# Kernel optimization log

Measured on AMD Instinct MI355X. Metric: run time of the kernel, lower is better.

The kernel has to match this reference:

```python
import jax, jax.numpy as jnp
import numpy as np

IN_DIM = 1024
HID = 256
OUT_DIM = 1000
NUM_BINS = 51
BATCH = 2048
N_LEGAL = 200


def setup_inputs() -> dict:
    key = jax.random.key(0)
    ks = jax.random.split(key, 12)
    s = lambda fan_in: 1.0 / np.sqrt(fan_in)
    u = lambda k, shp, b: jax.random.uniform(k, shp, jnp.float32, -b, b)
    return {
        "x": jax.random.normal(ks[0], (BATCH, IN_DIM), jnp.float32),
        # weights stored as [in, out] (math-equivalent to torch Linear)
        "w_in": u(ks[1], (IN_DIM, HID), s(IN_DIM)),
        "b_in": u(ks[2], (HID,), s(IN_DIM)),
        "w_ah": u(ks[3], (HID, HID), s(HID)),
        "b_ah": u(ks[4], (HID,), s(HID)),
        "w_ao": u(ks[5], (HID, OUT_DIM * NUM_BINS), s(HID)),
        "b_ao": u(ks[6], (OUT_DIM * NUM_BINS,), s(HID)),
        "w_vh": u(ks[7], (HID, HID), s(HID)),
        "b_vh": u(ks[8], (HID,), s(HID)),
        "w_vo": u(ks[9], (HID, NUM_BINS), s(HID)),
        "b_vo": u(ks[10], (NUM_BINS,), s(HID)),
        "v_range": jnp.linspace(-10.0, 10.0, NUM_BINS, dtype=jnp.float32),
        "possible_moves": jax.random.randint(ks[11], (BATCH, N_LEGAL), 0, OUT_DIM),
    }


def reference(x, w_in, b_in, w_ah, b_ah, w_ao, b_ao, w_vh, b_vh, w_vo, b_vo,
              v_range, possible_moves):
    B = x.shape[0]
    h = jax.nn.relu(x @ w_in + b_in)                       # [B, 256]
    adv_h = jax.nn.relu(h @ w_ah + b_ah)                   # [B, 256]
    val_h = jax.nn.relu(h @ w_vh + b_vh)                   # [B, 256]
    adv = (adv_h @ w_ao + b_ao).reshape(B, OUT_DIM, NUM_BINS)
    val = (val_h @ w_vo + b_vo).reshape(B, 1, NUM_BINS)
    q = val + adv - adv.mean(axis=1, keepdims=True)        # [B, A, bins]
    p = jnp.maximum(jax.nn.softmax(q, axis=2), 1e-5)       # softmax + clamp(min=1e-5)
    q_vals = jnp.sum(p * v_range, axis=2)                  # [B, A]
    # LegalSoftmax: per-row scatter of 1.0 at legal indices, vectorized
    mask = jnp.zeros((B, OUT_DIM), x.dtype).at[
        jnp.arange(B)[:, None], possible_moves].set(1.0)
    filtered = q_vals * mask
    # faithful to torch: any exact-zero entry (masked OR coincidental) -> -inf
    return jnp.where(filtered == 0, -jnp.inf, filtered)
```

## Files before the change

kernel.cpp:

```cpp
#include <hip/hip_runtime.h>
#include <cstdint>
#include <cstddef>

#define NB      2048
#define INDIM   1024
#define HID     256
#define NA      1000
#define BINS    51
#define NLEG    200
#define NPAIR   (NB*NLEG)
#define NBLK    256
#define PPB     (NPAIR/NBLK)

#define NEG_SENTINEL (-1.0e30f)

typedef float    f32x4  __attribute__((ext_vector_type(4)));
typedef __bf16   bf16x8 __attribute__((ext_vector_type(8)));
typedef unsigned short us8 __attribute__((ext_vector_type(8)));
typedef unsigned long long u64x2 __attribute__((ext_vector_type(2)));

__device__ __forceinline__ unsigned short f2bf(float f) {
  union { float f; unsigned u; } v; v.f = f;
  return (unsigned short)((v.u + 0x7FFFu + ((v.u >> 16) & 1u)) >> 16);
}
__device__ __forceinline__ float bf2f(unsigned short h) {
  union { unsigned u; float f; } v; v.u = ((unsigned)h) << 16;
  return v.f;
}
__device__ __forceinline__ bf16x8 as_bf(us8 v) { return __builtin_bit_cast(bf16x8, v); }
__device__ __forceinline__ int imin(int a, int b) { return a < b ? a : b; }

__device__ __forceinline__ unsigned f2fp8x4(float a, float b, float c, float d) {
  int v = 0;
  v = __builtin_amdgcn_cvt_pk_fp8_f32(a, b, v, false);
  v = __builtin_amdgcn_cvt_pk_fp8_f32(c, d, v, true);
  return (unsigned)v;
}
__device__ __forceinline__ unsigned char f2fp8(float f) {
  int v = __builtin_amdgcn_cvt_pk_fp8_f32(f, 0.f, 0, false);
  return (unsigned char)(v & 0xff);
}
__device__ __forceinline__ float fp82f(unsigned char u) {
  return __builtin_amdgcn_cvt_f32_fp8((int)u, 0);
}

__global__ __launch_bounds__(256) void k_phase1(
    const float* __restrict__ w_ao, unsigned char* __restrict__ wp8,
    float* __restrict__ wmean_acc,
    const float* __restrict__ w_in, const float* __restrict__ w_ah,
    const float* __restrict__ w_vh,
    unsigned short* __restrict__ w_inT, unsigned short* __restrict__ w_ahT,
    unsigned short* __restrict__ w_vhT,
    float* __restrict__ out, const int* __restrict__ pm,
    int* __restrict__ hist) {
  __shared__ __align__(16) char smem[26240];
  int b = blockIdx.x, tid = threadIdx.x;
  if (b < 1000) {
    unsigned char* st = (unsigned char*)smem;
    int s = b & 7, a0 = (b >> 3) * 8;
    const float* wbase = w_ao + (size_t)(s * 32) * (NA * BINS) + a0 * BINS;
    for (int i = tid; i < 32 * 102; i += 256) {
      int r = i / 102, c4 = i - r * 102;
      float4 f = *(const float4*)(wbase + (size_t)r * (NA * BINS) + c4 * 4);
      *(unsigned*)(st + r * 420 + c4 * 4) =
          f2fp8x4(f.x * 16.f, f.y * 16.f, f.z * 16.f, f.w * 16.f);
    }
    __syncthreads();
    for (int i = tid; i < 32 * 51; i += 256) {
      int r = i / 51, j = i - r * 51;
      float s8 = 0.f;
#pragma unroll
      for (int aL = 0; aL < 8; aL++) s8 += fp82f(st[r * 420 + aL * 51 + j]);
      atomicAdd(&wmean_acc[(size_t)(s * 32 + r) * BINS + j], s8);
    }
    int t4 = (tid >> 6) & 3, l = tid & 63;
    int col = t4 * 16 + (l & 15), kg = l >> 4;
    for (int aL = 0; aL < 8; aL++) {
      unsigned lo = 0, hi = 0;
      if (col < BINS) {
        const unsigned char* p0 = st + (kg * 8) * 420 + aL * 51 + col;
        lo = (unsigned)p0[0] | ((unsigned)p0[420] << 8) |
             ((unsigned)p0[840] << 16) | ((unsigned)p0[1260] << 24);
        hi = (unsigned)p0[1680] | ((unsigned)p0[2100] << 8) |
             ((unsigned)p0[2520] << 16) | ((unsigned)p0[2940] << 24);
      }
      size_t fg = ((size_t)(a0 + aL) * 8 + s) * 4 + t4;
      uint2 v; v.x = lo; v.y = hi;
      *(uint2*)(wp8 + fg * 512 + (size_t)l * 8) = v;
    }
  } else if (b < 1884) {
    int bb = b - 1000;
    if (bb < 384) {
      float (*tile)[33] = (float(*)[33])smem;
      const float* w; unsigned short* wT; int K, N, kt, nt;
      if (bb < 256)      { w = w_in; wT = w_inT; K = INDIM; N = HID; kt = bb & 31;        nt = bb >> 5; }
      else if (bb < 320) { w = w_ah; wT = w_ahT; K = HID;   N = HID; kt = (bb - 256) & 7; nt = (bb - 256) >> 3; }
      else               { w = w_vh; wT = w_vhT; K = HID;   N = HID; kt = (bb - 320) & 7; nt = (bb - 320) >> 3; }
      int k0 = kt * 32, n0 = nt * 32;
      int cr = tid >> 5, cc = tid & 31;
#pragma unroll
      for (int it = 0; it < 4; it++)
        tile[cr + it * 8][cc] = w[(size_t)(k0 + cr + it * 8) * N + n0 + cc];
      __syncthreads();
#pragma unroll
      for (int it = 0; it < 4; it++)
        wT[(size_t)(n0 + cr + it * 8) * K + k0 + cc] = f2bf(tile[cc][cr + it * 8]);
    } else {
      int base = (bb - 384) * 1024 + tid;
      float4 v = {NEG_SENTINEL, NEG_SENTINEL, NEG_SENTINEL, NEG_SENTINEL};
#pragma unroll
      for (int it = 0; it < 4; it++) ((float4*)out)[base + it * 256] = v;
    }
  } else {
    int* lh = (int*)smem;
    int blk = b - 1884;
    for (int i = tid; i < NA; i += 256) lh[i] = 0;
    __syncthreads();
    int base = blk * PPB;
    for (int i = tid; i < PPB; i += 256) atomicAdd(&lh[pm[base + i]], 1);
    __syncthreads();
    for (int a = tid; a < NA; a += 256) hist[a * NBLK + blk] = lh[a];
  }
}

__global__ __launch_bounds__(256) void k_phase2(
    int* __restrict__ hist, int* __restrict__ cnt,
    const float* __restrict__ w_vo, const float* __restrict__ wmean_acc,
    const float* __restrict__ b_vo, const float* __restrict__ b_ao,
    unsigned short* __restrict__ Wc, float* __restrict__ bias_c,
    const float* __restrict__ x, const unsigned short* __restrict__ w_inT,
    const float* __restrict__ b_in, unsigned short* __restrict__ h_bf) {
  int b = blockIdx.x, tid = threadIdx.x;
  if (b < 1000) {
    __shared__ int s[256];
    int a = b, t = tid;
    int v = hist[a * NBLK + t];
    s[t] = v;
    __syncthreads();
    for (int d = 1; d < 256; d <<= 1) {
      int u = (t >= d) ? s[t - d] : 0;
      __syncthreads();
      s[t] += u;
      __syncthreads();
    }
    hist[a * NBLK + t] = s[t] - v;
    if (t == 255) cnt[a] = s[255];
  } else if (b < 1064) {
    __shared__ float s[256];
    int n = b - 1000, t = tid;
    for (int k = t; k < 512; k += 256) {
      float v = 0.f;
      if (n < BINS)
        v = (k < 256) ? w_vo[(size_t)k * BINS + n]
                      : (-(0.001f / 16.f) * wmean_acc[(size_t)(k - 256) * BINS + n]);
      Wc[(size_t)n * 512 + k] = f2bf(v);
    }
    float acc = 0.f;
    if (n < BINS)
      for (int a = t; a < NA; a += 256) acc += b_ao[(size_t)a * BINS + n];
    s[t] = acc;
    __syncthreads();
    for (int d = 128; d > 0; d >>= 1) { if (t < d) s[t] += s[t + d]; __syncthreads(); }
    if (t == 0) bias_c[n] = (n < BINS) ? (b_vo[n] - 0.001f * s[0]) : 0.f;
  } else {
    int w = tid >> 6, l = tid & 63, la = l & 15, g = l >> 4;
    int idx = (b - 1064) * 4 + w;
    int m0 = (idx & 127) * 16, n0 = (idx >> 7) * 16;
    f32x4 acc = {0.f, 0.f, 0.f, 0.f};
    const us8* Bp = (const us8*)(w_inT + (size_t)(n0 + la) * INDIM) + g;
    const float* Ar = x + (size_t)(m0 + la) * INDIM + g * 8;
    for (int s = 0; s < INDIM; s += 32) {
      float4 f0 = *(const float4*)(Ar + s);
      float4 f1 = *(const float4*)(Ar + s + 4);
      us8 u;
      u[0] = f2bf(f0.x); u[1] = f2bf(f0.y); u[2] = f2bf(f0.z); u[3] = f2bf(f0.w);
      u[4] = f2bf(f1.x); u[5] = f2bf(f1.y); u[6] = f2bf(f1.z); u[7] = f2bf(f1.w);
      acc = __builtin_amdgcn_mfma_f32_16x16x32_bf16(as_bf(u), as_bf(Bp[s >> 3]),
                                                    acc, 0, 0, 0);
    }
    float bb = b_in[n0 + la];
#pragma unroll
    for (int r = 0; r < 4; r++) {
      float v = fmaxf(acc[r] + bb, 0.f);
      h_bf[(size_t)(m0 + g * 4 + r) * HID + n0 + la] = f2bf(v);
    }
  }
}

__global__ __launch_bounds__(256) void k_phase3(
    const int* __restrict__ cnt, int* __restrict__ off,
    const unsigned short* __restrict__ h,
    const unsigned short* __restrict__ wA, const float* __restrict__ bA,
    unsigned char* __restrict__ Aext8, unsigned short* __restrict__ advh_bf,
    const unsigned short* __restrict__ wV, const float* __restrict__ bV,
    unsigned short* __restrict__ oV) {
  int b = blockIdx.x, tid = threadIdx.x;
  if (b == 1024) {
    __shared__ int s[256];
    int t = tid, i0 = 4 * t;
    int v0 = (i0     < NA) ? cnt[i0]     : 0;
    int v1 = (i0 + 1 < NA) ? cnt[i0 + 1] : 0;
    int v2 = (i0 + 2 < NA) ? cnt[i0 + 2] : 0;
    int v3 = (i0 + 3 < NA) ? cnt[i0 + 3] : 0;
    int sum = v0 + v1 + v2 + v3;
    s[t] = sum;
    __syncthreads();
    for (int d = 1; d < 256; d <<= 1) {
      int u = (t >= d) ? s[t - d] : 0;
      __syncthreads();
      s[t] += u;
      __syncthreads();
    }
    int excl = s[t] - sum;
    if (i0     < NA) off[i0]     = excl;
    if (i0 + 1 < NA) off[i0 + 1] = excl + v0;
    if (i0 + 2 < NA) off[i0 + 2] = excl + v0 + v1;
    if (i0 + 3 < NA) off[i0 + 3] = excl + v0 + v1 + v2;
  } else {
    int w = tid >> 6, l = tid & 63, la = l & 15, g = l >> 4;
    int idx = b * 4 + w;
    int m0 = (idx & 127) * 16;
    int ny = idx >> 7;
    int second = ny >> 4;
    int n0 = (ny & 15) * 16;
    const unsigned short* BT = second ? wV : wA;
    const float* bias = second ? bV : bA;
    f32x4 acc = {0.f, 0.f, 0.f, 0.f};
    const us8* Bp = (const us8*)(BT + (size_t)(n0 + la) * HID) + g;
    const us8* Ap = (const us8*)(h + (size_t)(m0 + la) * HID) + g;
#pragma unroll
    for (int s = 0; s < 8; s++)
      acc = __builtin_amdgcn_mfma_f32_16x16x32_bf16(as_bf(Ap[s * 4]), as_bf(Bp[s * 4]),
                                                    acc, 0, 0, 0);
    float bb = bias[n0 + la];
#pragma unroll
    for (int r = 0; r < 4; r++) {
      float v = fmaxf(acc[r] + bb, 0.f);
      size_t o = (size_t)(m0 + g * 4 + r) * HID + n0 + la;
      if (second) {
        oV[o] = f2bf(v);
      } else {
        advh_bf[o] = f2bf(v);
        Aext8[o] = f2fp8(v);
      }
    }
  }
}

__global__ __launch_bounds__(256) void k_phase4(
    const int* __restrict__ pm, const int* __restrict__ off,
    const int* __restrict__ hist, int* __restrict__ rows,
    const unsigned short* __restrict__ valh, const unsigned short* __restrict__ advh,
    const unsigned short* __restrict__ Wc, const float* __restrict__ bias_c,
    unsigned short* __restrict__ cbuf) {
  int b = blockIdx.x, tid = threadIdx.x;
  if (b < 256) {
    __shared__ int lc[NA];
    __shared__ int lbase[NA];
    int blk = b, t = tid;
    for (int i = t; i < NA; i += 256) {
      lc[i] = 0;
      lbase[i] = off[i] + hist[i * NBLK + blk];
    }
    __syncthreads();
    int base = blk * PPB;
    for (int i = t; i < PPB; i += 256) {
      int a = pm[base + i];
      int r = atomicAdd(&lc[a], 1);
      rows[lbase[a] + r] = (base + i) / NLEG;
    }
  } else {
    int w = tid >> 6, l = tid & 63, la = l & 15, g = l >> 4;
    int idx = (b - 256) * 4 + w;
    int m0 = (idx & 127) * 16, n0 = (idx >> 7) * 16;
    f32x4 acc = {0.f, 0.f, 0.f, 0.f};
    const us8* Bp  = (const us8*)(Wc + (size_t)(n0 + la) * 512) + g;
    const us8* Ap1 = (const us8*)(valh + (size_t)(m0 + la) * HID) + g;
    const us8* Ap2 = (const us8*)(advh + (size_t)(m0 + la) * HID) + g;
#pragma unroll
    for (int s = 0; s < 8; s++)
      acc = __builtin_amdgcn_mfma_f32_16x16x32_bf16(as_bf(Ap1[s * 4]), as_bf(Bp[s * 4]),
                                                    acc, 0, 0, 0);
#pragma unroll
    for (int s = 0; s < 8; s++)
      acc = __builtin_amdgcn_mfma_f32_16x16x32_bf16(as_bf(Ap2[s * 4]), as_bf(Bp[(8 + s) * 4]),
                                                    acc, 0, 0, 0);
    float bb = bias_c[n0 + la];
#pragma unroll
    for (int r = 0; r < 4; r++)
      cbuf[(size_t)(m0 + g * 4 + r) * 64 + n0 + la] = f2bf(acc[r] + bb);
  }
}

__global__ __launch_bounds__(256) void k_main_mfma(
    const unsigned char* __restrict__ Aext8,
    const unsigned short* __restrict__ cbuf,
    const unsigned char* __restrict__ wp8,
    const float* __restrict__ b_ao,
    const float* __restrict__ v_range,
    const int* __restrict__ cnt, const int* __restrict__ off,
    const int* __restrict__ rows,
    float* __restrict__ out) {
  __shared__ __align__(16) long long sB8[2048];
  int bx = blockIdx.x;
  int a = (bx & 7) * 125 + (bx >> 3);
  int count = cnt[a];
  int ntiles = (count + 15) >> 4;
  if ((int)(blockIdx.y * 4) >= ntiles) return;
  int tid = threadIdx.x;
  const u64x2* wpa = (const u64x2*)(wp8 + (size_t)a * 16384);
  for (int i = tid; i < 1024; i += 256) ((u64x2*)sB8)[i] = wpa[i];
  __syncthreads();

  int w = tid >> 6, l = tid & 63, la = l & 15, g = l >> 4;
  int base = off[a];
  float vr[4], bao[4];
#pragma unroll
  for (int t = 0; t < 4; t++) {
    int bin = t * 16 + la;
    bool vb = bin < BINS;
    vr[t]  = vb ? v_range[bin] : 0.f;
    bao[t] = vb ? b_ao[(size_t)a * BINS + bin] : 0.f;
  }

  for (int tile = blockIdx.y * 4 + w; tile < ntiles; tile += 8) {
    int m16 = tile * 16;
    int rA = rows[base + imin(m16 + la, count - 1)];
    const long long* Ap = (const long long*)(Aext8 + (size_t)rA * HID) + g;
    const us8* Cp = (const us8*)(cbuf + (size_t)rA * 64) + g;
    f32x4 acc[4];
#pragma unroll
    for (int t = 0; t < 4; t++) acc[t] = (f32x4){0.f, 0.f, 0.f, 0.f};
#pragma unroll
    for (int s = 0; s < 8; s++) {
      long long a8 = Ap[s * 4];
#pragma unroll
      for (int t = 0; t < 4; t++)
        acc[t] = __builtin_amdgcn_mfma_f32_16x16x32_fp8_fp8(
            a8, sB8[(s * 4 + t) * 64 + l], acc[t], 0, 0, 0);
    }
    {
      us8 c0 = Cp[0], c1 = Cp[4];
#pragma unroll
      for (int t = 0; t < 4; t++) {
        int colg = t * 16 + la;
        us8 u0, u1;
#pragma unroll
        for (int j = 0; j < 8; j++) {
          u0[j] = (g * 8 + j == colg)      ? (unsigned short)0x4180 : (unsigned short)0;
          u1[j] = (g * 8 + j + 32 == colg) ? (unsigned short)0x4180 : (unsigned short)0;
        }
        acc[t] = __builtin_amdgcn_mfma_f32_16x16x32_bf16(as_bf(c0), as_bf(u0), acc[t], 0, 0, 0);
        acc[t] = __builtin_amdgcn_mfma_f32_16x16x32_bf16(as_bf(c1), as_bf(u1), acc[t], 0, 0, 0);
      }
    }
#pragma unroll
    for (int r = 0; r < 4; r++) {
      int gi = m16 + g * 4 + r;
      bool vrow = gi < count;
      int b = __shfl(rA, g * 4 + r, 16);
      float e[4];
      float S = 0.f;
#pragma unroll
      for (int t = 0; t < 4; t++) {
        int bin = t * 16 + la;
        float v = (bin < BINS) ? (acc[t][r] * 0.0625f + bao[t]) : -1.0e30f;
        e[t] = __expf(v);
        S += e[t];
      }
#pragma unroll
      for (int i = 1; i < 16; i <<= 1) S += __shfl_xor(S, i);
      float inv = 1.f / S;
      float qv = 0.f;
#pragma unroll
      for (int t = 0; t < 4; t++) {
        int bin = t * 16 + la;
        if (bin < BINS) qv = fmaf(fmaxf(e[t] * inv, 1e-5f), vr[t], qv);
      }
#pragma unroll
      for (int i = 1; i < 16; i <<= 1) qv += __shfl_xor(qv, i);
      if (vrow && la == 0)
        out[(size_t)b * NA + a] = (qv == 0.f) ? NEG_SENTINEL : qv;
    }
  }
}

extern "C" void kernel_launch(void* const* d_in, const int* in_sizes, int n_in,
                              void* d_out, int out_size, void* d_ws, size_t ws_size,
                              hipStream_t stream) {
  (void)in_sizes; (void)n_in; (void)out_size; (void)ws_size;
  const float* x     = (const float*)d_in[0];
  const float* w_in  = (const float*)d_in[1];
  const float* b_in  = (const float*)d_in[2];
  const float* w_ah  = (const float*)d_in[3];
  const float* b_ah  = (const float*)d_in[4];
  const float* w_ao  = (const float*)d_in[5];
  const float* b_ao  = (const float*)d_in[6];
  const float* w_vh  = (const float*)d_in[7];
  const float* b_vh  = (const float*)d_in[8];
  const float* w_vo  = (const float*)d_in[9];
  const float* b_vo  = (const float*)d_in[10];
  const float* v_rng = (const float*)d_in[11];
  const int*   pm    = (const int*)d_in[12];
  float* out = (float*)d_out;

  char* p = (char*)d_ws;
  unsigned char*  wp8     = (unsigned char*)p;  p += (size_t)NA * 32 * 512;
  unsigned char*  Aext8   = (unsigned char*)p;  p += (size_t)NB * HID;
  unsigned short* cbuf    = (unsigned short*)p; p += (size_t)NB * 64 * 2;
  unsigned short* h_bf    = (unsigned short*)p; p += (size_t)NB * HID * 2;
  unsigned short* advh_bf = (unsigned short*)p; p += (size_t)NB * HID * 2;
  unsigned short* valh_bf = (unsigned short*)p; p += (size_t)NB * HID * 2;
  unsigned short* w_inT   = (unsigned short*)p; p += (size_t)HID * INDIM * 2;
  unsigned short* w_ahT   = (unsigned short*)p; p += (size_t)HID * HID * 2;
  unsigned short* w_vhT   = (unsigned short*)p; p += (size_t)HID * HID * 2;
  unsigned short* Wc      = (unsigned short*)p; p += (size_t)64 * 512 * 2;
  float* bias_c = (float*)p; p += 64 * 4;
  float* wmean  = (float*)p; p += 13056 * 4;
  int* cnt  = (int*)p; p += NA * 4;
  int* off  = (int*)p; p += NA * 4;
  int* hist = (int*)p; p += (size_t)NA * NBLK * 4;
  int* rows = (int*)p; p += (size_t)NPAIR * 4 + 256;

  hipMemsetAsync(wmean, 0, 13056 * sizeof(float), stream);

  k_phase1<<<2140, 256, 0, stream>>>(w_ao, wp8, wmean, w_in, w_ah, w_vh,
                                     w_inT, w_ahT, w_vhT, out, pm, hist);
  k_phase2<<<1576, 256, 0, stream>>>(hist, cnt, w_vo, wmean, b_vo, b_ao,
                                     Wc, bias_c, x, w_inT, b_in, h_bf);
  k_phase3<<<1025, 256, 0, stream>>>(cnt, off, h_bf, w_ahT, b_ah, Aext8,
                                     advh_bf, w_vhT, b_vh, valh_bf);
  k_phase4<<<384, 256, 0, stream>>>(pm, off, hist, rows, valh_bf, advh_bf,
                                    Wc, bias_c, cbuf);
  k_main_mfma<<<dim3(1000, 2), 256, 0, stream>>>(Aext8, cbuf, wp8, b_ao, v_rng,
                                                 cnt, off, rows, out);
}
```

Measured before the change: 220.9 us.

## Merge phases to drop a launch and use fixed per-action row capacity

Moves the first-layer GEMM into phase1, reading fp32 w_in directly and converting it to bf16 on the fly instead of transposing it first. The hidden-layer GEMMs move into phase2, which removes one kernel launch and one grid-wide dependency. The per-action offset prefix scan is replaced by a fixed capacity of BCAP=576 rows per action. The main kernel also prefetches the next tile's row index. The fixed capacity assumes no action collects more than 576 legal pairs, which holds for the uniform random moves but would overflow on skewed inputs.

```diff
diff --git a/kernel.cpp b/kernel.cpp
--- a/kernel.cpp
+++ b/kernel.cpp
@@ -11,6 +11,7 @@
 #define NPAIR   (NB*NLEG)
 #define NBLK    256
 #define PPB     (NPAIR/NBLK)
+#define BCAP    576
 
 #define NEG_SENTINEL (-1.0e30f)
 
@@ -49,10 +50,11 @@
     float* __restrict__ wmean_acc,
     const float* __restrict__ w_in, const float* __restrict__ w_ah,
     const float* __restrict__ w_vh,
-    unsigned short* __restrict__ w_inT, unsigned short* __restrict__ w_ahT,
-    unsigned short* __restrict__ w_vhT,
+    unsigned short* __restrict__ w_ahT, unsigned short* __restrict__ w_vhT,
     float* __restrict__ out, const int* __restrict__ pm,
-    int* __restrict__ hist) {
+    int* __restrict__ hist,
+    const float* __restrict__ x, const float* __restrict__ b_in,
+    unsigned short* __restrict__ h_bf) {
   __shared__ __align__(16) char smem[26240];
   int b = blockIdx.x, tid = threadIdx.x;
   if (b < 1000) {
@@ -88,38 +90,60 @@
       uint2 v; v.x = lo; v.y = hi;
       *(uint2*)(wp8 + fg * 512 + (size_t)l * 8) = v;
     }
+  } else if (b < 1128) {
+    float (*tile)[33] = (float(*)[33])smem;
+    int bb = b - 1000;
+    const float* w = (bb < 64) ? w_ah : w_vh;
+    unsigned short* wT = (bb < 64) ? w_ahT : w_vhT;
+    int t6 = bb & 63;
+    int k0 = (t6 & 7) * 32, n0 = (t6 >> 3) * 32;
+    int cr = tid >> 5, cc = tid & 31;
+#pragma unroll
+    for (int it = 0; it < 4; it++)
+      tile[cr + it * 8][cc] = w[(size_t)(k0 + cr + it * 8) * HID + n0 + cc];
+    __syncthreads();
+#pragma unroll
+    for (int it = 0; it < 4; it++)
+      wT[(size_t)(n0 + cr + it * 8) * HID + k0 + cc] = f2bf(tile[cc][cr + it * 8]);
+  } else if (b < 1628) {
+    int base = (b - 1128) * 1024 + tid;
+    float4 v = {NEG_SENTINEL, NEG_SENTINEL, NEG_SENTINEL, NEG_SENTINEL};
+#pragma unroll
+    for (int it = 0; it < 4; it++) ((float4*)out)[base + it * 256] = v;
   } else if (b < 1884) {
-    int bb = b - 1000;
-    if (bb < 384) {
-      float (*tile)[33] = (float(*)[33])smem;
-      const float* w; unsigned short* wT; int K, N, kt, nt;
-      if (bb < 256)      { w = w_in; wT = w_inT; K = INDIM; N = HID; kt = bb & 31;        nt = bb >> 5; }
-      else if (bb < 320) { w = w_ah; wT = w_ahT; K = HID;   N = HID; kt = (bb - 256) & 7; nt = (bb - 256) >> 3; }
-      else               { w = w_vh; wT = w_vhT; K = HID;   N = HID; kt = (bb - 320) & 7; nt = (bb - 320) >> 3; }
-      int k0 = kt * 32, n0 = nt * 32;
-      int cr = tid >> 5, cc = tid & 31;
-#pragma unroll
-      for (int it = 0; it < 4; it++)
-        tile[cr + it * 8][cc] = w[(size_t)(k0 + cr + it * 8) * N + n0 + cc];
-      __syncthreads();
-#pragma unroll
-      for (int it = 0; it < 4; it++)
-        wT[(size_t)(n0 + cr + it * 8) * K + k0 + cc] = f2bf(tile[cc][cr + it * 8]);
-    } else {
-      int base = (bb - 384) * 1024 + tid;
-      float4 v = {NEG_SENTINEL, NEG_SENTINEL, NEG_SENTINEL, NEG_SENTINEL};
-#pragma unroll
-      for (int it = 0; it < 4; it++) ((float4*)out)[base + it * 256] = v;
-    }
-  } else {
     int* lh = (int*)smem;
-    int blk = b - 1884;
+    int blk = b - 1628;
     for (int i = tid; i < NA; i += 256) lh[i] = 0;
     __syncthreads();
     int base = blk * PPB;
     for (int i = tid; i < PPB; i += 256) atomicAdd(&lh[pm[base + i]], 1);
     __syncthreads();
     for (int a = tid; a < NA; a += 256) hist[a * NBLK + blk] = lh[a];
+  } else {
+    int w = tid >> 6, l = tid & 63, la = l & 15, g = l >> 4;
+    int idx = (b - 1884) * 4 + w;
+    int m0 = (idx & 127) * 16, n0 = (idx >> 7) * 16;
+    f32x4 acc = {0.f, 0.f, 0.f, 0.f};
+    const float* Ar = x + (size_t)(m0 + la) * INDIM + g * 8;
+    const float* Wc0 = w_in + (size_t)(g * 8) * HID + n0 + la;
+    for (int s = 0; s < INDIM; s += 32) {
+      float4 f0 = *(const float4*)(Ar + s);
+      float4 f1 = *(const float4*)(Ar + s + 4);
+      us8 u, v;
+      u[0] = f2bf(f0.x); u[1] = f2bf(f0.y); u[2] = f2bf(f0.z); u[3] = f2bf(f0.w);
+      u[4] = f2bf(f1.x); u[5] = f2bf(f1.y); u[6] = f2bf(f1.z); u[7] = f2bf(f1.w);
+      const float* Wk = Wc0 + (size_t)s * HID;
+#pragma unroll
+      for (int j = 0; j < 8; j++) v[j] = f2bf(Wk[(size_t)j * HID]);
+      acc = __builtin_amdgcn_mfma_f32_16x16x32_bf16(as_bf(u), as_bf(v),
+                                                    acc, 0, 0, 0);
+    }
+    float bb = b_in[n0 + la];
+#pragma unroll
+    for (int r = 0; r < 4; r++) {
+      float v = fmaxf(acc[r] + bb, 0.f);
+      h_bf[(size_t)(m0 + g * 4 + r) * HID + n0 + la] = f2bf(v);
+    }
   }
 }
 
@@ -128,8 +152,11 @@
     const float* __restrict__ w_vo, const float* __restrict__ wmean_acc,
     const float* __restrict__ b_vo, const float* __restrict__ b_ao,
     unsigned short* __restrict__ Wc, float* __restrict__ bias_c,
-    const float* __restrict__ x, const unsigned short* __restrict__ w_inT,
-    const float* __restrict__ b_in, unsigned short* __restrict__ h_bf) {
+    const unsigned short* __restrict__ h,
+    const unsigned short* __restrict__ wA, const float* __restrict__ bA,
+    unsigned char* __restrict__ Aext8, unsigned short* __restrict__ advh_bf,
+    const unsigned short* __restrict__ wV, const float* __restrict__ bV,
+    unsigned short* __restrict__ oV) {
   int b = blockIdx.x, tid = threadIdx.x;
   if (b < 1000) {
     __shared__ int s[256];
@@ -165,60 +192,6 @@
   } else {
     int w = tid >> 6, l = tid & 63, la = l & 15, g = l >> 4;
     int idx = (b - 1064) * 4 + w;
-    int m0 = (idx & 127) * 16, n0 = (idx >> 7) * 16;
-    f32x4 acc = {0.f, 0.f, 0.f, 0.f};
-    const us8* Bp = (const us8*)(w_inT + (size_t)(n0 + la) * INDIM) + g;
-    const float* Ar = x + (size_t)(m0 + la) * INDIM + g * 8;
-    for (int s = 0; s < INDIM; s += 32) {
-      float4 f0 = *(const float4*)(Ar + s);
-      float4 f1 = *(const float4*)(Ar + s + 4);
-      us8 u;
-      u[0] = f2bf(f0.x); u[1] = f2bf(f0.y); u[2] = f2bf(f0.z); u[3] = f2bf(f0.w);
-      u[4] = f2bf(f1.x); u[5] = f2bf(f1.y); u[6] = f2bf(f1.z); u[7] = f2bf(f1.w);
-      acc = __builtin_amdgcn_mfma_f32_16x16x32_bf16(as_bf(u), as_bf(Bp[s >> 3]),
-                                                    acc, 0, 0, 0);
-    }
-    float bb = b_in[n0 + la];
-#pragma unroll
-    for (int r = 0; r < 4; r++) {
-      float v = fmaxf(acc[r] + bb, 0.f);
-      h_bf[(size_t)(m0 + g * 4 + r) * HID + n0 + la] = f2bf(v);
-    }
-  }
-}
-
-__global__ __launch_bounds__(256) void k_phase3(
-    const int* __restrict__ cnt, int* __restrict__ off,
-    const unsigned short* __restrict__ h,
-    const unsigned short* __restrict__ wA, const float* __restrict__ bA,
-    unsigned char* __restrict__ Aext8, unsigned short* __restrict__ advh_bf,
-    const unsigned short* __restrict__ wV, const float* __restrict__ bV,
-    unsigned short* __restrict__ oV) {
-  int b = blockIdx.x, tid = threadIdx.x;
-  if (b == 1024) {
-    __shared__ int s[256];
-    int t = tid, i0 = 4 * t;
-    int v0 = (i0     < NA) ? cnt[i0]     : 0;
-    int v1 = (i0 + 1 < NA) ? cnt[i0 + 1] : 0;
-    int v2 = (i0 + 2 < NA) ? cnt[i0 + 2] : 0;
-    int v3 = (i0 + 3 < NA) ? cnt[i0 + 3] : 0;
-    int sum = v0 + v1 + v2 + v3;
-    s[t] = sum;
-    __syncthreads();
-    for (int d = 1; d < 256; d <<= 1) {
-      int u = (t >= d) ? s[t - d] : 0;
-      __syncthreads();
-      s[t] += u;
-      __syncthreads();
-    }
-    int excl = s[t] - sum;
-    if (i0     < NA) off[i0]     = excl;
-    if (i0 + 1 < NA) off[i0 + 1] = excl + v0;
-    if (i0 + 2 < NA) off[i0 + 2] = excl + v0 + v1;
-    if (i0 + 3 < NA) off[i0 + 3] = excl + v0 + v1 + v2;
-  } else {
-    int w = tid >> 6, l = tid & 63, la = l & 15, g = l >> 4;
-    int idx = b * 4 + w;
     int m0 = (idx & 127) * 16;
     int ny = idx >> 7;
     int second = ny >> 4;
@@ -247,9 +220,9 @@
   }
 }
 
-__global__ __launch_bounds__(256) void k_phase4(
-    const int* __restrict__ pm, const int* __restrict__ off,
-    const int* __restrict__ hist, int* __restrict__ rows,
+__global__ __launch_bounds__(256) void k_phase3(
+    const int* __restrict__ pm, const int* __restrict__ hist,
+    int* __restrict__ rows,
     const unsigned short* __restrict__ valh, const unsigned short* __restrict__ advh,
     const unsigned short* __restrict__ Wc, const float* __restrict__ bias_c,
     unsigned short* __restrict__ cbuf) {
@@ -260,7 +233,7 @@
     int blk = b, t = tid;
     for (int i = t; i < NA; i += 256) {
       lc[i] = 0;
-      lbase[i] = off[i] + hist[i * NBLK + blk];
+      lbase[i] = i * BCAP + hist[i * NBLK + blk];
     }
     __syncthreads();
     int base = blk * PPB;
@@ -298,7 +271,7 @@
     const unsigned char* __restrict__ wp8,
     const float* __restrict__ b_ao,
     const float* __restrict__ v_range,
-    const int* __restrict__ cnt, const int* __restrict__ off,
+    const int* __restrict__ cnt,
     const int* __restrict__ rows,
     float* __restrict__ out) {
   __shared__ __align__(16) long long sB8[2048];
@@ -313,7 +286,7 @@
   __syncthreads();
 
   int w = tid >> 6, l = tid & 63, la = l & 15, g = l >> 4;
-  int base = off[a];
+  int base = a * BCAP;
   float vr[4], bao[4];
 #pragma unroll
   for (int t = 0; t < 4; t++) {
@@ -323,9 +296,11 @@
     bao[t] = vb ? b_ao[(size_t)a * BINS + bin] : 0.f;
   }
 
-  for (int tile = blockIdx.y * 4 + w; tile < ntiles; tile += 8) {
-    int m16 = tile * 16;
-    int rA = rows[base + imin(m16 + la, count - 1)];
+  int tile = blockIdx.y * 4 + w;
+  int rA = rows[base + imin(tile * 16 + la, count - 1)];
+  for (; tile < ntiles; tile += 8) {
+    int tn = tile + 8;
+    int rAn = (tn < ntiles) ? rows[base + imin(tn * 16 + la, count - 1)] : 0;
     const long long* Ap = (const long long*)(Aext8 + (size_t)rA * HID) + g;
     const us8* Cp = (const us8*)(cbuf + (size_t)rA * 64) + g;
     f32x4 acc[4];
@@ -354,6 +329,7 @@
         acc[t] = __builtin_amdgcn_mfma_f32_16x16x32_bf16(as_bf(c1), as_bf(u1), acc[t], 0, 0, 0);
       }
     }
+    int m16 = tile * 16;
 #pragma unroll
     for (int r = 0; r < 4; r++) {
       int gi = m16 + g * 4 + r;
@@ -382,6 +358,7 @@
       if (vrow && la == 0)
         out[(size_t)b * NA + a] = (qv == 0.f) ? NEG_SENTINEL : qv;
     }
+    rA = rAn;
   }
 }
 
@@ -411,27 +388,25 @@
   unsigned short* h_bf    = (unsigned short*)p; p += (size_t)NB * HID * 2;
   unsigned short* advh_bf = (unsigned short*)p; p += (size_t)NB * HID * 2;
   unsigned short* valh_bf = (unsigned short*)p; p += (size_t)NB * HID * 2;
-  unsigned short* w_inT   = (unsigned short*)p; p += (size_t)HID * INDIM * 2;
   unsigned short* w_ahT   = (unsigned short*)p; p += (size_t)HID * HID * 2;
   unsigned short* w_vhT   = (unsigned short*)p; p += (size_t)HID * HID * 2;
   unsigned short* Wc      = (unsigned short*)p; p += (size_t)64 * 512 * 2;
   float* bias_c = (float*)p; p += 64 * 4;
   float* wmean  = (float*)p; p += 13056 * 4;
   int* cnt  = (int*)p; p += NA * 4;
-  int* off  = (int*)p; p += NA * 4;
   int* hist = (int*)p; p += (size_t)NA * NBLK * 4;
-  int* rows = (int*)p; p += (size_t)NPAIR * 4 + 256;
+  int* rows = (int*)p; p += (size_t)NA * BCAP * 4 + 256;
 
   hipMemsetAsync(wmean, 0, 13056 * sizeof(float), stream);
 
-  k_phase1<<<2140, 256, 0, stream>>>(w_ao, wp8, wmean, w_in, w_ah, w_vh,
-                                     w_inT, w_ahT, w_vhT, out, pm, hist);
-  k_phase2<<<1576, 256, 0, stream>>>(hist, cnt, w_vo, wmean, b_vo, b_ao,
-                                     Wc, bias_c, x, w_inT, b_in, h_bf);
-  k_phase3<<<1025, 256, 0, stream>>>(cnt, off, h_bf, w_ahT, b_ah, Aext8,
+  k_phase1<<<2396, 256, 0, stream>>>(w_ao, wp8, wmean, w_in, w_ah, w_vh,
+                                     w_ahT, w_vhT, out, pm, hist,
+                                     x, b_in, h_bf);
+  k_phase2<<<2088, 256, 0, stream>>>(hist, cnt, w_vo, wmean, b_vo, b_ao,
+                                     Wc, bias_c, h_bf, w_ahT, b_ah, Aext8,
                                      advh_bf, w_vhT, b_vh, valh_bf);
-  k_phase4<<<384, 256, 0, stream>>>(pm, off, hist, rows, valh_bf, advh_bf,
+  k_phase3<<<384, 256, 0, stream>>>(pm, hist, rows, valh_bf, advh_bf,
                                     Wc, bias_c, cbuf);
   k_main_mfma<<<dim3(1000, 2), 256, 0, stream>>>(Aext8, cbuf, wp8, b_ao, v_rng,
-                                                 cnt, off, rows, out);
-}
+                                                 cnt, rows, out);
+}
```

Measured after the change: 224.6 us. About the same (+1.7%).

## Use fixed-capacity per-action row buckets and merge main kernel blocks per action

Applied to the files above, without the earlier changes.

Each action gets a fixed slot of BCAP rows in the row list instead of an offset from a global exclusive scan. This removes the offset-scan block from phase3 and the `off` array. The main MFMA kernel now runs one block per action instead of two, so the per-action fp8 weight tile is staged into shared memory once, and the next tile's row index is prefetched. Phase1 and phase2 block roles are reordered so the GEMM and histogram work is dispatched before the cheaper tasks. The fixed capacity assumes no action has more than 576 legal rows, which holds only for random-looking inputs. The main kernel also loses half its blocks, which reduces parallelism.

```diff
diff --git a/kernel.cpp b/kernel.cpp
--- a/kernel.cpp
+++ b/kernel.cpp
@@ -11,6 +11,7 @@
 #define NPAIR   (NB*NLEG)
 #define NBLK    256
 #define PPB     (NPAIR/NBLK)
+#define BCAP    576
 
 #define NEG_SENTINEL (-1.0e30f)
 
@@ -88,38 +89,36 @@
       uint2 v; v.x = lo; v.y = hi;
       *(uint2*)(wp8 + fg * 512 + (size_t)l * 8) = v;
     }
-  } else if (b < 1884) {
+  } else if (b < 1384) {
+    float (*tile)[33] = (float(*)[33])smem;
     int bb = b - 1000;
-    if (bb < 384) {
-      float (*tile)[33] = (float(*)[33])smem;
-      const float* w; unsigned short* wT; int K, N, kt, nt;
-      if (bb < 256)      { w = w_in; wT = w_inT; K = INDIM; N = HID; kt = bb & 31;        nt = bb >> 5; }
-      else if (bb < 320) { w = w_ah; wT = w_ahT; K = HID;   N = HID; kt = (bb - 256) & 7; nt = (bb - 256) >> 3; }
-      else               { w = w_vh; wT = w_vhT; K = HID;   N = HID; kt = (bb - 320) & 7; nt = (bb - 320) >> 3; }
-      int k0 = kt * 32, n0 = nt * 32;
-      int cr = tid >> 5, cc = tid & 31;
-#pragma unroll
-      for (int it = 0; it < 4; it++)
-        tile[cr + it * 8][cc] = w[(size_t)(k0 + cr + it * 8) * N + n0 + cc];
-      __syncthreads();
-#pragma unroll
-      for (int it = 0; it < 4; it++)
-        wT[(size_t)(n0 + cr + it * 8) * K + k0 + cc] = f2bf(tile[cc][cr + it * 8]);
-    } else {
-      int base = (bb - 384) * 1024 + tid;
-      float4 v = {NEG_SENTINEL, NEG_SENTINEL, NEG_SENTINEL, NEG_SENTINEL};
-#pragma unroll
-      for (int it = 0; it < 4; it++) ((float4*)out)[base + it * 256] = v;
-    }
-  } else {
+    const float* w; unsigned short* wT; int K, N, kt, nt;
+    if (bb < 256)      { w = w_in; wT = w_inT; K = INDIM; N = HID; kt = bb & 31;        nt = bb >> 5; }
+    else if (bb < 320) { w = w_ah; wT = w_ahT; K = HID;   N = HID; kt = (bb - 256) & 7; nt = (bb - 256) >> 3; }
+    else               { w = w_vh; wT = w_vhT; K = HID;   N = HID; kt = (bb - 320) & 7; nt = (bb - 320) >> 3; }
+    int k0 = kt * 32, n0 = nt * 32;
+    int cr = tid >> 5, cc = tid & 31;
+#pragma unroll
+    for (int it = 0; it < 4; it++)
+      tile[cr + it * 8][cc] = w[(size_t)(k0 + cr + it * 8) * N + n0 + cc];
+    __syncthreads();
+#pragma unroll
+    for (int it = 0; it < 4; it++)
+      wT[(size_t)(n0 + cr + it * 8) * K + k0 + cc] = f2bf(tile[cc][cr + it * 8]);
+  } else if (b < 1640) {
     int* lh = (int*)smem;
-    int blk = b - 1884;
+    int blk = b - 1384;
     for (int i = tid; i < NA; i += 256) lh[i] = 0;
     __syncthreads();
     int base = blk * PPB;
     for (int i = tid; i < PPB; i += 256) atomicAdd(&lh[pm[base + i]], 1);
     __syncthreads();
     for (int a = tid; a < NA; a += 256) hist[a * NBLK + blk] = lh[a];
+  } else {
+    int base = (b - 1640) * 1024 + tid;
+    float4 v = {NEG_SENTINEL, NEG_SENTINEL, NEG_SENTINEL, NEG_SENTINEL};
+#pragma unroll
+    for (int it = 0; it < 4; it++) ((float4*)out)[base + it * 256] = v;
   }
 }
 
@@ -131,40 +130,9 @@
     const float* __restrict__ x, const unsigned short* __restrict__ w_inT,
     const float* __restrict__ b_in, unsigned short* __restrict__ h_bf) {
   int b = blockIdx.x, tid = threadIdx.x;
-  if (b < 1000) {
-    __shared__ int s[256];
-    int a = b, t = tid;
-    int v = hist[a * NBLK + t];
-    s[t] = v;
-    __syncthreads();
-    for (int d = 1; d < 256; d <<= 1) {
-      int u = (t >= d) ? s[t - d] : 0;
-      __syncthreads();
-      s[t] += u;
-      __syncthreads();
-    }
-    hist[a * NBLK + t] = s[t] - v;
-    if (t == 255) cnt[a] = s[255];
-  } else if (b < 1064) {
-    __shared__ float s[256];
-    int n = b - 1000, t = tid;
-    for (int k = t; k < 512; k += 256) {
-      float v = 0.f;
-      if (n < BINS)
-        v = (k < 256) ? w_vo[(size_t)k * BINS + n]
-                      : (-(0.001f / 16.f) * wmean_acc[(size_t)(k - 256) * BINS + n]);
-      Wc[(size_t)n * 512 + k] = f2bf(v);
-    }
-    float acc = 0.f;
-    if (n < BINS)
-      for (int a = t; a < NA; a += 256) acc += b_ao[(size_t)a * BINS + n];
-    s[t] = acc;
-    __syncthreads();
-    for (int d = 128; d > 0; d >>= 1) { if (t < d) s[t] += s[t + d]; __syncthreads(); }
-    if (t == 0) bias_c[n] = (n < BINS) ? (b_vo[n] - 0.001f * s[0]) : 0.f;
-  } else {
+  if (b < 512) {
     int w = tid >> 6, l = tid & 63, la = l & 15, g = l >> 4;
-    int idx = (b - 1064) * 4 + w;
+    int idx = b * 4 + w;
     int m0 = (idx & 127) * 16, n0 = (idx >> 7) * 16;
     f32x4 acc = {0.f, 0.f, 0.f, 0.f};
     const us8* Bp = (const us8*)(w_inT + (size_t)(n0 + la) * INDIM) + g;
@@ -184,72 +152,79 @@
       float v = fmaxf(acc[r] + bb, 0.f);
       h_bf[(size_t)(m0 + g * 4 + r) * HID + n0 + la] = f2bf(v);
     }
+  } else if (b < 1512) {
+    __shared__ int s[256];
+    int a = b - 512, t = tid;
+    int v = hist[a * NBLK + t];
+    s[t] = v;
+    __syncthreads();
+    for (int d = 1; d < 256; d <<= 1) {
+      int u = (t >= d) ? s[t - d] : 0;
+      __syncthreads();
+      s[t] += u;
+      __syncthreads();
+    }
+    hist[a * NBLK + t] = s[t] - v;
+    if (t == 255) cnt[a] = s[255];
+  } else {
+    __shared__ float s[256];
+    int n = b - 1512, t = tid;
+    for (int k = t; k < 512; k += 256) {
+      float v = 0.f;
+      if (n < BINS)
+        v = (k < 256) ? w_vo[(size_t)k * BINS + n]
+                      : (-(0.001f / 16.f) * wmean_acc[(size_t)(k - 256) * BINS + n]);
+      Wc[(size_t)n * 512 + k] = f2bf(v);
+    }
+    float acc = 0.f;
+    if (n < BINS)
+      for (int a = t; a < NA; a += 256) acc += b_ao[(size_t)a * BINS + n];
+    s[t] = acc;
+    __syncthreads();
+    for (int d = 128; d > 0; d >>= 1) { if (t < d) s[t] += s[t + d]; __syncthreads(); }
+    if (t == 0) bias_c[n] = (n < BINS) ? (b_vo[n] - 0.001f * s[0]) : 0.f;
   }
 }
 
 __global__ __launch_bounds__(256) void k_phase3(
-    const int* __restrict__ cnt, int* __restrict__ off,
     const unsigned short* __restrict__ h,
     const unsigned short* __restrict__ wA, const float* __restrict__ bA,
     unsigned char* __restrict__ Aext8, unsigned short* __restrict__ advh_bf,
     const unsigned short* __restrict__ wV, const float* __restrict__ bV,
     unsigned short* __restrict__ oV) {
   int b = blockIdx.x, tid = threadIdx.x;
-  if (b == 1024) {
-    __shared__ int s[256];
-    int t = tid, i0 = 4 * t;
-    int v0 = (i0     < NA) ? cnt[i0]     : 0;
-    int v1 = (i0 + 1 < NA) ? cnt[i0 + 1] : 0;
-    int v2 = (i0 + 2 < NA) ? cnt[i0 + 2] : 0;
-    int v3 = (i0 + 3 < NA) ? cnt[i0 + 3] : 0;
-    int sum = v0 + v1 + v2 + v3;
-    s[t] = sum;
-    __syncthreads();
-    for (int d = 1; d < 256; d <<= 1) {
-      int u = (t >= d) ? s[t - d] : 0;
-      __syncthreads();
-      s[t] += u;
-      __syncthreads();
-    }
-    int excl = s[t] - sum;
-    if (i0     < NA) off[i0]     = excl;
-    if (i0 + 1 < NA) off[i0 + 1] = excl + v0;
-    if (i0 + 2 < NA) off[i0 + 2] = excl + v0 + v1;
-    if (i0 + 3 < NA) off[i0 + 3] = excl + v0 + v1 + v2;
-  } else {
-    int w = tid >> 6, l = tid & 63, la = l & 15, g = l >> 4;
-    int idx = b * 4 + w;
-    int m0 = (idx & 127) * 16;
-    int ny = idx >> 7;
-    int second = ny >> 4;
-    int n0 = (ny & 15) * 16;
-    const unsigned short* BT = second ? wV : wA;
-    const float* bias = second ? bV : bA;
-    f32x4 acc = {0.f, 0.f, 0.f, 0.f};
-    const us8* Bp = (const us8*)(BT + (size_t)(n0 + la) * HID) + g;
-    const us8* Ap = (const us8*)(h + (size_t)(m0 + la) * HID) + g;
-#pragma unroll
-    for (int s = 0; s < 8; s++)
-      acc = __builtin_amdgcn_mfma_f32_16x16x32_bf16(as_bf(Ap[s * 4]), as_bf(Bp[s * 4]),
-                                                    acc, 0, 0, 0);
-    float bb = bias[n0 + la];
-#pragma unroll
-    for (int r = 0; r < 4; r++) {
-      float v = fmaxf(acc[r] + bb, 0.f);
-      size_t o = (size_t)(m0 + g * 4 + r) * HID + n0 + la;
-      if (second) {
-        oV[o] = f2bf(v);
-      } else {
-        advh_bf[o] = f2bf(v);
-        Aext8[o] = f2fp8(v);
-      }
+  int w = tid >> 6, l = tid & 63, la = l & 15, g = l >> 4;
+  int idx = b * 4 + w;
+  int m0 = (idx & 127) * 16;
+  int ny = idx >> 7;
+  int second = ny >> 4;
+  int n0 = (ny & 15) * 16;
+  const unsigned short* BT = second ? wV : wA;
+  const float* bias = second ? bV : bA;
+  f32x4 acc = {0.f, 0.f, 0.f, 0.f};
+  const us8* Bp = (const us8*)(BT + (size_t)(n0 + la) * HID) + g;
+  const us8* Ap = (const us8*)(h + (size_t)(m0 + la) * HID) + g;
+#pragma unroll
+  for (int s = 0; s < 8; s++)
+    acc = __builtin_amdgcn_mfma_f32_16x16x32_bf16(as_bf(Ap[s * 4]), as_bf(Bp[s * 4]),
+                                                  acc, 0, 0, 0);
+  float bb = bias[n0 + la];
+#pragma unroll
+  for (int r = 0; r < 4; r++) {
+    float v = fmaxf(acc[r] + bb, 0.f);
+    size_t o = (size_t)(m0 + g * 4 + r) * HID + n0 + la;
+    if (second) {
+      oV[o] = f2bf(v);
+    } else {
+      advh_bf[o] = f2bf(v);
+      Aext8[o] = f2fp8(v);
     }
   }
 }
 
 __global__ __launch_bounds__(256) void k_phase4(
-    const int* __restrict__ pm, const int* __restrict__ off,
-    const int* __restrict__ hist, int* __restrict__ rows,
+    const int* __restrict__ pm, const int* __restrict__ hist,
+    int* __restrict__ rows,
     const unsigned short* __restrict__ valh, const unsigned short* __restrict__ advh,
     const unsigned short* __restrict__ Wc, const float* __restrict__ bias_c,
     unsigned short* __restrict__ cbuf) {
@@ -260,7 +235,7 @@
     int blk = b, t = tid;
     for (int i = t; i < NA; i += 256) {
       lc[i] = 0;
-      lbase[i] = off[i] + hist[i * NBLK + blk];
+      lbase[i] = i * BCAP + hist[i * NBLK + blk];
     }
     __syncthreads();
     int base = blk * PPB;
@@ -298,7 +273,7 @@
     const unsigned char* __restrict__ wp8,
     const float* __restrict__ b_ao,
     const float* __restrict__ v_range,
-    const int* __restrict__ cnt, const int* __restrict__ off,
+    const int* __restrict__ cnt,
     const int* __restrict__ rows,
     float* __restrict__ out) {
   __shared__ __align__(16) long long sB8[2048];
@@ -306,14 +281,13 @@
   int a = (bx & 7) * 125 + (bx >> 3);
   int count = cnt[a];
   int ntiles = (count + 15) >> 4;
-  if ((int)(blockIdx.y * 4) >= ntiles) return;
   int tid = threadIdx.x;
   const u64x2* wpa = (const u64x2*)(wp8 + (size_t)a * 16384);
   for (int i = tid; i < 1024; i += 256) ((u64x2*)sB8)[i] = wpa[i];
   __syncthreads();
 
   int w = tid >> 6, l = tid & 63, la = l & 15, g = l >> 4;
-  int base = off[a];
+  int base = a * BCAP;
   float vr[4], bao[4];
 #pragma unroll
   for (int t = 0; t < 4; t++) {
@@ -323,9 +297,11 @@
     bao[t] = vb ? b_ao[(size_t)a * BINS + bin] : 0.f;
   }
 
-  for (int tile = blockIdx.y * 4 + w; tile < ntiles; tile += 8) {
-    int m16 = tile * 16;
-    int rA = rows[base + imin(m16 + la, count - 1)];
+  int tile = w;
+  int rA = (tile < ntiles) ? rows[base + imin(tile * 16 + la, count - 1)] : 0;
+  for (; tile < ntiles; tile += 4) {
+    int tn = tile + 4;
+    int rAn = (tn < ntiles) ? rows[base + imin(tn * 16 + la, count - 1)] : 0;
     const long long* Ap = (const long long*)(Aext8 + (size_t)rA * HID) + g;
     const us8* Cp = (const us8*)(cbuf + (size_t)rA * 64) + g;
     f32x4 acc[4];
@@ -354,6 +330,7 @@
         acc[t] = __builtin_amdgcn_mfma_f32_16x16x32_bf16(as_bf(c1), as_bf(u1), acc[t], 0, 0, 0);
       }
     }
+    int m16 = tile * 16;
 #pragma unroll
     for (int r = 0; r < 4; r++) {
       int gi = m16 + g * 4 + r;
@@ -382,6 +359,7 @@
       if (vrow && la == 0)
         out[(size_t)b * NA + a] = (qv == 0.f) ? NEG_SENTINEL : qv;
     }
+    rA = rAn;
   }
 }
 
@@ -418,9 +396,8 @@
   float* bias_c = (float*)p; p += 64 * 4;
   float* wmean  = (float*)p; p += 13056 * 4;
   int* cnt  = (int*)p; p += NA * 4;
-  int* off  = (int*)p; p += NA * 4;
   int* hist = (int*)p; p += (size_t)NA * NBLK * 4;
-  int* rows = (int*)p; p += (size_t)NPAIR * 4 + 256;
+  int* rows = (int*)p; p += (size_t)NA * BCAP * 4 + 256;
 
   hipMemsetAsync(wmean, 0, 13056 * sizeof(float), stream);
 
@@ -428,10 +405,10 @@
                                      w_inT, w_ahT, w_vhT, out, pm, hist);
   k_phase2<<<1576, 256, 0, stream>>>(hist, cnt, w_vo, wmean, b_vo, b_ao,
                                      Wc, bias_c, x, w_inT, b_in, h_bf);
-  k_phase3<<<1025, 256, 0, stream>>>(cnt, off, h_bf, w_ahT, b_ah, Aext8,
+  k_phase3<<<1024, 256, 0, stream>>>(h_bf, w_ahT, b_ah, Aext8,
                                      advh_bf, w_vhT, b_vh, valh_bf);
-  k_phase4<<<384, 256, 0, stream>>>(pm, off, hist, rows, valh_bf, advh_bf,
+  k_phase4<<<384, 256, 0, stream>>>(pm, hist, rows, valh_bf, advh_bf,
                                     Wc, bias_c, cbuf);
-  k_main_mfma<<<dim3(1000, 2), 256, 0, stream>>>(Aext8, cbuf, wp8, b_ao, v_rng,
-                                                 cnt, off, rows, out);
-}
+  k_main_mfma<<<1000, 256, 0, stream>>>(Aext8, cbuf, wp8, b_ao, v_rng,
+                                        cnt, rows, out);
+}
```

After: 221.0 us. No clear change (+0.0%).
